# Kernel tuning notes

Hardware: AMD Instinct MI355X
Metric: run time of the kernel (lower is better)

## Reference

```python
import jax, jax.numpy as jnp
import numpy as np

B, S, V = 16, 256, 32000
E, H, L, FFN, NC = 256, 8, 2, 1024, 4
DK = E // H
NQ = E  # n_qubits == hidden_dim == embed_dim (required by the module's shape constraints)
EPS = 1e-5


def qproj(x, theta):
    # Analytic simulation of: RX(x_k) encode + trainable RX(theta_k) + CNOT ladder + MeasureAll(PauliZ).
    # RX gates on the same wire compose; CNOT ladder maps Z_j -> Z_0...Z_j in Heisenberg picture, so
    # <Z_j> = prod_{k<=j} cos(x_k + theta_k)  (product state expectation).
    return jnp.cumprod(jnp.cos(x + theta), axis=-1)


def layernorm(x, g, b):
    m = x.mean(-1, keepdims=True)
    v = x.var(-1, keepdims=True)
    return (x - m) * jax.lax.rsqrt(v + EPS) * g + b


def sinusoidal_pe(seq, d):
    pos = jnp.arange(seq, dtype=jnp.float32)[:, None]
    div = jnp.exp(jnp.arange(0, d, 2, dtype=jnp.float32) * (-np.log(10000.0) / d))
    pe = jnp.zeros((seq, d), jnp.float32)
    pe = pe.at[:, 0::2].set(jnp.sin(pos * div)).at[:, 1::2].set(jnp.cos(pos * div))
    return pe


def _forward(x, token_emb, lstm_W, lstm_b, lstm_theta, ln1_g, ln1_b, ln2_g, ln2_b,
             qkv_theta, combine_W, combine_b, ffn_theta, lin1_W, lin1_b, lin2_W, lin2_b,
             cls_W, cls_b):
    emb = token_emb[x]  # (B, S, E)

    # --- QLSTM: each gate = linear -> quantum circuit -> nonlinearity ---
    def step(carry, xt):
        hx, cx = carry
        comb = jnp.concatenate([xt, hx], axis=-1)                      # (B, 2E)
        z = jnp.einsum('bd,gdq->gbq', comb, lstm_W) + lstm_b[:, None]  # (4, B, NQ)
        q = jnp.cumprod(jnp.cos(z + lstm_theta[:, None, :]), axis=-1)
        f = jax.nn.sigmoid(q[0])
        i = jax.nn.sigmoid(q[1])
        g = jnp.tanh(q[2])
        o = jax.nn.sigmoid(q[3])
        cx = f * cx + i * g
        hx = o * jnp.tanh(cx)
        return (hx, cx), hx

    h0 = jnp.zeros((emb.shape[0], NQ), emb.dtype)
    _, hs = jax.lax.scan(step, (h0, h0), jnp.swapaxes(emb, 0, 1))
    h = jnp.swapaxes(hs, 0, 1)  # (B, S, NQ)

    h = h + sinusoidal_pe(h.shape[1], E)[None]

    # --- quantum transformer blocks ---
    def heads(t):
        return t.reshape(t.shape[0], t.shape[1], H, DK).transpose(0, 2, 1, 3)

    for l in range(L):
        q = qproj(h, qkv_theta[l, 0])
        k = qproj(h, qkv_theta[l, 1])
        v = qproj(h, qkv_theta[l, 2])
        qh, kh, vh = heads(q), heads(k), heads(v)
        scores = jnp.einsum('bhqd,bhkd->bhqk', qh, kh) / jnp.sqrt(jnp.float32(DK))
        attn = jax.nn.softmax(scores, axis=-1)
        out = jnp.einsum('bhqk,bhkd->bhqd', attn, vh).transpose(0, 2, 1, 3).reshape(h.shape)
        out = out @ combine_W[l] + combine_b[l]
        h = layernorm(h + out, ln1_g[l], ln1_b[l])
        ff = qproj(h, ffn_theta[l]) @ lin1_W[l] + lin1_b[l]
        ff = jax.nn.relu(ff) @ lin2_W[l] + lin2_b[l]
        h = layernorm(h + ff, ln2_g[l], ln2_b[l])

    pooled = h.mean(axis=1)  # (B, E)
    return pooled @ cls_W + cls_b  # (B, NC)


def setup_inputs() -> dict:
    key = jax.random.key(0)
    ks = jax.random.split(key, 10)
    s = 0.05
    return {
        'x': jax.random.randint(ks[0], (B, S), 0, V),
        'token_emb': jax.random.normal(ks[1], (V, E), jnp.float32) * s,
        'lstm_W': jax.random.normal(ks[2], (4, 2 * E, NQ), jnp.float32) * s,
        'lstm_b': jnp.zeros((4, NQ), jnp.float32),
        'lstm_theta': jax.random.normal(ks[3], (4, NQ), jnp.float32) * s,
        'ln1_g': jnp.ones((L, E), jnp.float32),
        'ln1_b': jnp.zeros((L, E), jnp.float32),
        'ln2_g': jnp.ones((L, E), jnp.float32),
        'ln2_b': jnp.zeros((L, E), jnp.float32),
        'qkv_theta': jax.random.normal(ks[4], (L, 3, E), jnp.float32) * s,
        'combine_W': jax.random.normal(ks[5], (L, E, E), jnp.float32) * s,
        'combine_b': jnp.zeros((L, E), jnp.float32),
        'ffn_theta': jax.random.normal(ks[6], (L, E), jnp.float32) * s,
        'lin1_W': jax.random.normal(ks[7], (L, E, FFN), jnp.float32) * s,
        'lin1_b': jnp.zeros((L, FFN), jnp.float32),
        'lin2_W': jax.random.normal(ks[8], (L, FFN, E), jnp.float32) * s,
        'lin2_b': jnp.zeros((L, E), jnp.float32),
        'cls_W': jax.random.normal(ks[9], (E, NC), jnp.float32) * s,
        'cls_b': jnp.zeros((NC,), jnp.float32),
    }


def reference(x, token_emb, lstm_W, lstm_b, lstm_theta, ln1_g, ln1_b, ln2_g, ln2_b,
              qkv_theta, combine_W, combine_b, ffn_theta, lin1_W, lin1_b, lin2_W, lin2_b,
              cls_W, cls_b):
    return _forward(x, token_emb, lstm_W, lstm_b, lstm_theta, ln1_g, ln1_b, ln2_g, ln2_b,
                    qkv_theta, combine_W, combine_b, ffn_theta, lin1_W, lin1_b, lin2_W, lin2_b,
                    cls_W, cls_b)
```

## Files before the change

kernel.cpp:

```cpp
#include <hip/hip_runtime.h>
#include <hip/hip_bf16.h>


typedef __attribute__((ext_vector_type(8))) short bf8v;
typedef __attribute__((ext_vector_type(4))) float f4v;
#define MFMA16 __builtin_amdgcn_mfma_f32_16x16x32_bf16

__device__ __forceinline__ unsigned short f2bf(float f) {
  unsigned u = __builtin_bit_cast(unsigned, f);
  u += 0x7fffu + ((u >> 16) & 1u);
  return (unsigned short)(u >> 16);
}
__device__ __forceinline__ float rcp_f(float x) { return __builtin_amdgcn_rcpf(x); }
__device__ __forceinline__ float sigm(float x) { return rcp_f(1.f + __expf(-x)); }
__device__ __forceinline__ float tanh_f(float x) { return 1.f - 2.f * rcp_f(__expf(2.f * x) + 1.f); }

#define DOT2BF(acc, a, b) \
  asm("v_dot2_f32_bf16 %0, %1, %2, %0" : "+v"(acc) : "v"(a), "v"(b))

__global__ void embed_kernel(const int* __restrict__ x, const float* __restrict__ tab,
                             unsigned short* __restrict__ eb) {
  int tok = blockIdx.x, tid = threadIdx.x;
  eb[tok * 256 + tid] = f2bf(tab[x[tok] * 256 + tid]);
}

__global__ void pack_bt(const float* __restrict__ W, int K, int N,
                        unsigned short* __restrict__ Th, long wz, long tz) {
  __shared__ float tile[64][65];
  W += (long)blockIdx.z * wz;
  Th += (long)blockIdx.z * tz;
  int n0 = blockIdx.x * 64, k0 = blockIdx.y * 64;
  int tid = threadIdx.x, tx = tid & 63, ty = tid >> 6;
  for (int r = ty; r < 64; r += 4) tile[r][tx] = W[(k0 + r) * N + n0 + tx];
  __syncthreads();
  for (int r = ty; r < 64; r += 4) {
    Th[(n0 + r) * K + k0 + tx] = f2bf(tile[tx][r]);
  }
}

__global__ void pack_wreg_kernel(const float* __restrict__ lstmW, unsigned* __restrict__ Wreg) {
  int o = blockIdx.x * 256 + threadIdx.x;
  int c = o & 3;
  int q = (o >> 2) & 255;
  int i4 = (o >> 10) & 7;
  int s = (o >> 13) & 3;
  int gi = o >> 15;
  int d = s * 64 + 2 * (i4 * 4 + c);
  unsigned lo = f2bf(lstmW[(gi * 512 + 256 + d) * 256 + q]);
  unsigned hi = f2bf(lstmW[(gi * 512 + 256 + d + 1) * 256 + q]);
  Wreg[o] = lo | (hi << 16);
}

__global__ void pack_wl_kernel(const float* __restrict__ lstmW, unsigned* __restrict__ WLg) {
  int o = blockIdx.x * 256 + threadIdx.x;
  int c = o & 3;
  int q = (o >> 2) & 255;
  int p4 = o >> 10;
  int d = 2 * (p4 * 4 + c);
  unsigned lo = f2bf(lstmW[(3 * 512 + 256 + d) * 256 + q]);
  unsigned hi = f2bf(lstmW[(3 * 512 + 256 + d + 1) * 256 + q]);
  WLg[o] = lo | (hi << 16);
}

__global__ void __launch_bounds__(256) gemm_mfma(const unsigned short* __restrict__ A,
                                                 const unsigned short* __restrict__ B,
                                                 const float* __restrict__ bias,
                                                 float* __restrict__ Cf,
                                                 unsigned short* __restrict__ Cb,
                                                 int M, int N, int K, int mode) {
  __shared__ unsigned short As[128 * 40];
  __shared__ unsigned short Bs[128 * 40];

  const int tid = threadIdx.x;
  const int lane = tid & 63;
  const int wid = tid >> 6;
  const int wr = wid >> 1, wc = wid & 1;
  const int bm = blockIdx.y * 128, bn = blockIdx.x * 128;

  const int srow = tid >> 2;
  const int scol = (tid & 3) * 8;

  f4v acc[4][4] = {};

  for (int kt = 0; kt < K; kt += 32) {
#pragma unroll
    for (int p = 0; p < 2; ++p) {
      int r = srow + p * 64;
      *(uint4*)(&As[r * 40 + scol]) = *(const uint4*)(&A[(bm + r) * K + kt + scol]);
      *(uint4*)(&Bs[r * 40 + scol]) = *(const uint4*)(&B[(bn + r) * K + kt + scol]);
    }
    __syncthreads();

    bf8v a[4], b[4];
    const int kq = (lane >> 4) * 8;
#pragma unroll
    for (int f = 0; f < 4; ++f) {
      a[f] = *(const bf8v*)(&As[(wr * 64 + f * 16 + (lane & 15)) * 40 + kq]);
      b[f] = *(const bf8v*)(&Bs[(wc * 64 + f * 16 + (lane & 15)) * 40 + kq]);
    }
#pragma unroll
    for (int fm = 0; fm < 4; ++fm)
#pragma unroll
      for (int fn = 0; fn < 4; ++fn)
        acc[fm][fn] = MFMA16(a[fm], b[fn], acc[fm][fn], 0, 0, 0);
    __syncthreads();
  }

#pragma unroll
  for (int fm = 0; fm < 4; ++fm)
#pragma unroll
    for (int fn = 0; fn < 4; ++fn) {
      int c = bn + wc * 64 + fn * 16 + (lane & 15);
      int r0 = bm + wr * 64 + fm * 16 + ((lane >> 4) << 2);
      float bv = bias[c];
#pragma unroll
      for (int j = 0; j < 4; ++j) {
        float v = acc[fm][fn][j] + bv;
        if (mode == 1) {
          Cb[(r0 + j) * N + c] = f2bf(fmaxf(v, 0.f));
        } else {
          Cf[(r0 + j) * N + c] = v;
        }
      }
    }
}

__global__ void __launch_bounds__(1024, 4) lstm_kernel(const unsigned* __restrict__ Wreg,
                                                       const unsigned* __restrict__ WLg,
                                                       const float* __restrict__ lstmTh,
                                                       const float* __restrict__ xw,
                                                       float* __restrict__ hb) {
  extern __shared__ char smem[];
  unsigned* WL = (unsigned*)smem;
  float* part = (float*)(smem + 131072);
  float* qv = part + 4096;
  float* wtot = qv + 1024;
  unsigned* hp = (unsigned*)(wtot + 16);

  const int t = threadIdx.x;
  const int b = blockIdx.x;
  const int q = t & 255;
  const int s = t >> 8;
  const int lane = t & 63;
  const int w = t >> 6;

  {
    const uint4* src = (const uint4*)WLg;
    uint4* dst = (uint4*)WL;
    for (int j = t; j < 8192; j += 1024) dst[j] = src[j];
  }
  const uint4* Wreg4 = (const uint4*)Wreg;
  uint4 wreg[24];
#pragma unroll
  for (int j = 0; j < 24; ++j) {
    int gi = j >> 3, i4 = j & 7;
    wreg[j] = Wreg4[((gi * 4 + s) * 8 + i4) * 256 + q];
  }
  const float th = lstmTh[t];
  float cx = 0.f;
  if (t < 128) hp[t] = 0u;
  __syncthreads();

  const int xbase = (b << 8) * 1024;
  const uint4* WL4 = (const uint4*)WL;
  const uint4* hp4 = (const uint4*)hp;

  for (int st = 0; st < 256; ++st) {
    float xv = xw[xbase + st * 1024 + t];

    float a0 = 0.f, a1 = 0.f, a2 = 0.f, a3 = 0.f;
#pragma unroll
    for (int i4 = 0; i4 < 8; ++i4) {
      uint4 hh = hp4[(s << 3) + i4];
      uint4 w3 = WL4[((s << 3) + i4) * 256 + q];
      uint4 w0 = wreg[i4];
      uint4 w1 = wreg[8 + i4];
      uint4 w2 = wreg[16 + i4];
      DOT2BF(a0, w0.x, hh.x); DOT2BF(a0, w0.y, hh.y);
      DOT2BF(a0, w0.z, hh.z); DOT2BF(a0, w0.w, hh.w);
      DOT2BF(a1, w1.x, hh.x); DOT2BF(a1, w1.y, hh.y);
      DOT2BF(a1, w1.z, hh.z); DOT2BF(a1, w1.w, hh.w);
      DOT2BF(a2, w2.x, hh.x); DOT2BF(a2, w2.y, hh.y);
      DOT2BF(a2, w2.z, hh.z); DOT2BF(a2, w2.w, hh.w);
      DOT2BF(a3, w3.x, hh.x); DOT2BF(a3, w3.y, hh.y);
      DOT2BF(a3, w3.z, hh.z); DOT2BF(a3, w3.w, hh.w);
    }
    part[(0 * 4 + s) * 256 + q] = a0;
    part[(1 * 4 + s) * 256 + q] = a1;
    part[(2 * 4 + s) * 256 + q] = a2;
    part[(3 * 4 + s) * 256 + q] = a3;
    __syncthreads();

    float z = part[(s * 4 + 0) * 256 + q] + part[(s * 4 + 1) * 256 + q] +
              part[(s * 4 + 2) * 256 + q] + part[(s * 4 + 3) * 256 + q] + xv + th;
    float v = __cosf(z);

#pragma unroll
    for (int off = 1; off < 64; off <<= 1) {
      float o = __shfl_up(v, off, 64);
      if (lane >= off) v *= o;
    }
    if (lane == 63) wtot[w] = v;
    __syncthreads();
    {
      float p = 1.f;
      int w0g = w & ~3;
      for (int k = w0g; k < w; ++k) p *= wtot[k];
      v *= p;
    }
    qv[t] = v;
    __syncthreads();

    if (t < 256) {
      float fg = sigm(qv[t]);
      float ig = sigm(qv[256 + t]);
      float gg = tanh_f(qv[512 + t]);
      float og = sigm(qv[768 + t]);
      cx = fg * cx + ig * gg;
      float hv = og * tanh_f(cx);
      hb[((b << 8) + st) * 256 + t] = hv;
      float nb = __shfl_xor(hv, 1, 64);
      if ((t & 1) == 0) hp[t >> 1] = (unsigned)f2bf(hv) | ((unsigned)f2bf(nb) << 16);
    }
    __syncthreads();
  }
}

__global__ void pe_add_kernel(float* __restrict__ h) {
  int tok = blockIdx.x, tid = threadIdx.x;
  int s = tok & 255;
  int j = tid >> 1;
  float div = __expf((float)j * -0.07195578415622253f);
  float ang = (float)s * div;
  float pe = (tid & 1) ? __cosf(ang) : __sinf(ang);
  h[tok * 256 + tid] += pe;
}

__global__ void qproj3_kernel(const float* __restrict__ hin, const float* __restrict__ thetas,
                              float* __restrict__ outbase) {
  __shared__ float wtot[4];
  int tok = blockIdx.x, y = blockIdx.y;
  int tid = threadIdx.x, lane = tid & 63, wid = tid >> 6;
  const float* theta = thetas + y * 256;
  float* out = outbase + (long)y * 1048576;
  float v = __cosf(hin[tok * 256 + tid] + theta[tid]);
#pragma unroll
  for (int off = 1; off < 64; off <<= 1) {
    float o = __shfl_up(v, off, 64);
    if (lane >= off) v *= o;
  }
  if (lane == 63) wtot[wid] = v;
  __syncthreads();
  float pre = 1.f;
  for (int w = 0; w < wid; ++w) pre *= wtot[w];
  out[tok * 256 + tid] = v * pre;
}

__global__ void qproj_bf_kernel(const float* __restrict__ hin, const float* __restrict__ theta,
                                unsigned short* __restrict__ outb) {
  __shared__ float wtot[4];
  int tok = blockIdx.x, tid = threadIdx.x, lane = tid & 63, wid = tid >> 6;
  float v = __cosf(hin[tok * 256 + tid] + theta[tid]);
#pragma unroll
  for (int off = 1; off < 64; off <<= 1) {
    float o = __shfl_up(v, off, 64);
    if (lane >= off) v *= o;
  }
  if (lane == 63) wtot[wid] = v;
  __syncthreads();
  float pre = 1.f;
  for (int w = 0; w < wid; ++w) pre *= wtot[w];
  outb[tok * 256 + tid] = f2bf(v * pre);
}

__global__ void __launch_bounds__(256, 1) attn_kernel(const float* __restrict__ qb,
                                                      const float* __restrict__ kb,
                                                      const float* __restrict__ vb,
                                                      unsigned short* __restrict__ outb) {
  extern __shared__ float sm[];
  float* Qs = sm;
  float* Ks = Qs + 256 * 33;
  float* Vs = Ks + 256 * 33;
  float* ps = Vs + 256 * 33;
  int hd = blockIdx.x, b = blockIdx.y;
  int tid = threadIdx.x, lane = tid & 63, wid = tid >> 6;
  const float scale = 0.17677669529663687f;

  for (int i = tid; i < 256 * 32; i += 256) {
    int r = i >> 5, d = i & 31;
    int src = (b * 256 + r) * 256 + hd * 32 + d;
    Qs[r * 33 + d] = qb[src];
    Ks[r * 33 + d] = kb[src];
    Vs[r * 33 + d] = vb[src];
  }
  __syncthreads();

  float* pw = ps + wid * 256;
  for (int r = wid; r < 256; r += 4) {
    float qreg[32];
#pragma unroll
    for (int d = 0; d < 32; ++d) qreg[d] = Qs[r * 33 + d];
    float s[4];
#pragma unroll
    for (int j = 0; j < 4; ++j) {
      int k = lane + 64 * j;
      float a = 0.f;
#pragma unroll
      for (int d = 0; d < 32; ++d) a += qreg[d] * Ks[k * 33 + d];
      s[j] = a * scale;
    }
    float m = fmaxf(fmaxf(s[0], s[1]), fmaxf(s[2], s[3]));
#pragma unroll
    for (int off = 32; off; off >>= 1) m = fmaxf(m, __shfl_xor(m, off, 64));
    float p[4], sum = 0.f;
#pragma unroll
    for (int j = 0; j < 4; ++j) { p[j] = __expf(s[j] - m); sum += p[j]; }
#pragma unroll
    for (int off = 32; off; off >>= 1) sum += __shfl_xor(sum, off, 64);
    float inv = rcp_f(sum);
#pragma unroll
    for (int j = 0; j < 4; ++j) pw[lane + 64 * j] = p[j] * inv;
    int d = lane & 31, half = lane >> 5;
    float a = 0.f;
#pragma unroll 8
    for (int i2 = 0; i2 < 128; ++i2) {
      int k = half * 128 + i2;
      a += pw[k] * Vs[k * 33 + d];
    }
    a += __shfl_down(a, 32, 64);
    if (lane < 32) outb[(b * 256 + r) * 256 + hd * 32 + d] = f2bf(a);
  }
}

__global__ void ln_kernel(float* __restrict__ hio, const float* __restrict__ delta,
                          const float* __restrict__ gamma, const float* __restrict__ beta) {
  __shared__ float red[16];
  int tok = blockIdx.x, tid = threadIdx.x, lane = tid & 63, wid = tid >> 6;
  float v = hio[tok * 256 + tid] + delta[tok * 256 + tid];
  float s1 = v, s2 = v * v;
#pragma unroll
  for (int off = 32; off; off >>= 1) {
    s1 += __shfl_xor(s1, off, 64);
    s2 += __shfl_xor(s2, off, 64);
  }
  if (lane == 0) { red[wid] = s1; red[wid + 8] = s2; }
  __syncthreads();
  float t1 = red[0] + red[1] + red[2] + red[3];
  float t2 = red[8] + red[9] + red[10] + red[11];
  float mean = t1 * (1.f / 256.f);
  float var = t2 * (1.f / 256.f) - mean * mean;
  float w = rsqrtf(var + 1e-5f);
  hio[tok * 256 + tid] = (v - mean) * w * gamma[tid] + beta[tid];
}

__global__ void pool_cls_kernel(const float* __restrict__ h, const float* __restrict__ clsW,
                                const float* __restrict__ clsb, float* __restrict__ out) {
  __shared__ float pl[256];
  __shared__ float red[8];
  int b = blockIdx.x, tid = threadIdx.x, lane = tid & 63, wid = tid >> 6;
  float s = 0.f;
  for (int t = 0; t < 256; ++t) s += h[(b * 256 + t) * 256 + tid];
  pl[tid] = s * (1.f / 256.f);
  __syncthreads();
  for (int c = 0; c < 4; ++c) {
    float v = pl[tid] * clsW[tid * 4 + c];
#pragma unroll
    for (int off = 32; off; off >>= 1) v += __shfl_xor(v, off, 64);
    if (lane == 0) red[wid] = v;
    __syncthreads();
    if (tid == 0) out[b * 4 + c] = red[0] + red[1] + red[2] + red[3] + clsb[c];
    __syncthreads();
  }
}

extern "C" void kernel_launch(void* const* d_in, const int* in_sizes, int n_in,
                              void* d_out, int out_size, void* d_ws, size_t ws_size,
                              hipStream_t stream) {
  const int* x = (const int*)d_in[0];
  const float* token_emb = (const float*)d_in[1];
  const float* lstm_W = (const float*)d_in[2];
  const float* lstm_b = (const float*)d_in[3];
  const float* lstm_th = (const float*)d_in[4];
  const float* ln1_g = (const float*)d_in[5];
  const float* ln1_b = (const float*)d_in[6];
  const float* ln2_g = (const float*)d_in[7];
  const float* ln2_b = (const float*)d_in[8];
  const float* qkv_th = (const float*)d_in[9];
  const float* comb_W = (const float*)d_in[10];
  const float* comb_b = (const float*)d_in[11];
  const float* ffn_th = (const float*)d_in[12];
  const float* lin1_W = (const float*)d_in[13];
  const float* lin1_b = (const float*)d_in[14];
  const float* lin2_W = (const float*)d_in[15];
  const float* lin2_b = (const float*)d_in[16];
  const float* cls_W = (const float*)d_in[17];
  const float* cls_b = (const float*)d_in[18];

  float* ws = (float*)d_ws;
  typedef unsigned short ushort_t;
  ushort_t* emb_b = (ushort_t*)ws;
  ushort_t* att_b = emb_b;
  float* xw = ws + 1048576;
  ushort_t* ffh_b = (ushort_t*)xw;
  float* hb = ws + 5242880;
  float* qq = ws + 6291456;
  float* kk = ws + 7340032;
  float* vv = ws + 8388608;
  float* tmp = ws + 9437184;
  unsigned* Wreg = (unsigned*)tmp;
  unsigned* WLg = (unsigned*)(tmp + 98304);
  ushort_t* ffq_b = (ushort_t*)(ws + 10485760);
  ushort_t* wxt_b = (ushort_t*)(ws + 11534336);
  ushort_t* cmb_b = wxt_b + 262144;
  ushort_t* l1_b = cmb_b + 131072;
  ushort_t* l2_b = l1_b + 524288;

  const int LSTM_LDS = 131072 + 16384 + 4096 + 64 + 512;
  const int ATT_LDS = (3 * 256 * 33 + 4 * 256) * 4;
  (void)hipFuncSetAttribute(reinterpret_cast<const void*>(lstm_kernel),
                            hipFuncAttributeMaxDynamicSharedMemorySize, LSTM_LDS);
  (void)hipFuncSetAttribute(reinterpret_cast<const void*>(attn_kernel),
                            hipFuncAttributeMaxDynamicSharedMemorySize, ATT_LDS);

  embed_kernel<<<4096, 256, 0, stream>>>(x, token_emb, emb_b);
  pack_wreg_kernel<<<384, 256, 0, stream>>>(lstm_W, Wreg);
  pack_wl_kernel<<<128, 256, 0, stream>>>(lstm_W, WLg);
  pack_bt<<<dim3(4, 4, 4), 256, 0, stream>>>(lstm_W, 256, 256, wxt_b, 131072, 65536);
  pack_bt<<<dim3(4, 4, 2), 256, 0, stream>>>(comb_W, 256, 256, cmb_b, 65536, 65536);
  pack_bt<<<dim3(16, 4, 2), 256, 0, stream>>>(lin1_W, 256, 1024, l1_b, 262144, 262144);
  pack_bt<<<dim3(4, 16, 2), 256, 0, stream>>>(lin2_W, 1024, 256, l2_b, 262144, 262144);

  gemm_mfma<<<dim3(8, 32), 256, 0, stream>>>(emb_b, wxt_b, lstm_b,
                                             xw, nullptr, 4096, 1024, 256, 0);
  lstm_kernel<<<16, 1024, LSTM_LDS, stream>>>(Wreg, WLg, lstm_th, xw, hb);
  pe_add_kernel<<<4096, 256, 0, stream>>>(hb);

  for (int l = 0; l < 2; ++l) {
    qproj3_kernel<<<dim3(4096, 3), 256, 0, stream>>>(hb, qkv_th + l * 768, qq);
    attn_kernel<<<dim3(8, 16), 256, ATT_LDS, stream>>>(qq, kk, vv, att_b);
    gemm_mfma<<<dim3(2, 32), 256, 0, stream>>>(att_b, cmb_b + l * 65536, comb_b + l * 256,
                                               tmp, nullptr, 4096, 256, 256, 0);
    ln_kernel<<<4096, 256, 0, stream>>>(hb, tmp, ln1_g + l * 256, ln1_b + l * 256);
    qproj_bf_kernel<<<4096, 256, 0, stream>>>(hb, ffn_th + l * 256, ffq_b);
    gemm_mfma<<<dim3(8, 32), 256, 0, stream>>>(ffq_b, l1_b + l * 262144, lin1_b + l * 1024,
                                               nullptr, ffh_b, 4096, 1024, 256, 1);
    gemm_mfma<<<dim3(2, 32), 256, 0, stream>>>(ffh_b, l2_b + l * 262144, lin2_b + l * 256,
                                               tmp, nullptr, 4096, 256, 1024, 0);
    ln_kernel<<<4096, 256, 0, stream>>>(hb, tmp, ln2_g + l * 256, ln2_b + l * 256);
  }

  pool_cls_kernel<<<16, 256, 0, stream>>>(hb, cls_W, cls_b, (float*)d_out);
}
```

Before: 1.427 ms.

## Halve LSTM block to 512 threads and vectorize attention LDS access

The recurrent LSTM kernel now runs 512 threads per batch, each holding twice the register-resident recurrent weights (48 uint4) and computing two gate outputs. This cuts the cross-K-slice partial reduction from four slices to two and folds the per-wave cumprod prefix into the gate stage, removing one barrier per timestep. The next step's input projection is prefetched during the current step. The attention kernel pads Q/K rows to 36 floats and transposes V so that dot products use float4 LDS loads. The LSTM change raises register pressure a lot and risks spills.

```diff
diff --git a/kernel.cpp b/kernel.cpp
--- a/kernel.cpp
+++ b/kernel.cpp
@@ -42,10 +42,11 @@
   int o = blockIdx.x * 256 + threadIdx.x;
   int c = o & 3;
   int q = (o >> 2) & 255;
-  int i4 = (o >> 10) & 7;
-  int s = (o >> 13) & 3;
-  int gi = o >> 15;
-  int d = s * 64 + 2 * (i4 * 4 + c);
+  int i4 = (o >> 10) & 15;
+  int gs = o >> 14;
+  int gi = gs >> 1, s = gs & 1;
+  int i = i4 * 4 + c;
+  int d = s * 128 + 2 * i;
   unsigned lo = f2bf(lstmW[(gi * 512 + 256 + d) * 256 + q]);
   unsigned hi = f2bf(lstmW[(gi * 512 + 256 + d + 1) * 256 + q]);
   Wreg[o] = lo | (hi << 16);
@@ -125,15 +126,17 @@
     }
 }
 
-__global__ void __launch_bounds__(1024, 4) lstm_kernel(const unsigned* __restrict__ Wreg,
-                                                       const unsigned* __restrict__ WLg,
-                                                       const float* __restrict__ lstmTh,
-                                                       const float* __restrict__ xw,
-                                                       float* __restrict__ hb) {
+__global__ void
+__attribute__((amdgpu_flat_work_group_size(512, 512), amdgpu_waves_per_eu(2, 2)))
+lstm_kernel(const unsigned* __restrict__ Wreg,
+            const unsigned* __restrict__ WLg,
+            const float* __restrict__ lstmTh,
+            const float* __restrict__ xw,
+            float* __restrict__ hb) {
   extern __shared__ char smem[];
   unsigned* WL = (unsigned*)smem;
   float* part = (float*)(smem + 131072);
-  float* qv = part + 4096;
+  float* qv = part + 2048;
   float* wtot = qv + 1024;
   unsigned* hp = (unsigned*)(wtot + 16);
 
@@ -147,16 +150,21 @@
   {
     const uint4* src = (const uint4*)WLg;
     uint4* dst = (uint4*)WL;
-    for (int j = t; j < 8192; j += 1024) dst[j] = src[j];
+    for (int j = t; j < 8192; j += 512) dst[j] = src[j];
   }
   const uint4* Wreg4 = (const uint4*)Wreg;
-  uint4 wreg[24];
-#pragma unroll
-  for (int j = 0; j < 24; ++j) {
-    int gi = j >> 3, i4 = j & 7;
-    wreg[j] = Wreg4[((gi * 4 + s) * 8 + i4) * 256 + q];
-  }
-  const float th = lstmTh[t];
+  uint4 wreg[48];
+#pragma unroll
+  for (int j = 0; j < 48; ++j) {
+    int gi = j >> 4, i4 = j & 15;
+    wreg[j] = Wreg4[((gi * 2 + s) * 16 + i4) * 256 + q];
+  }
+#pragma unroll
+  for (int j = 0; j < 48; ++j) {
+    asm volatile("" : "+v"(wreg[j].x), "+v"(wreg[j].y), "+v"(wreg[j].z), "+v"(wreg[j].w));
+  }
+  const float thA = lstmTh[t];
+  const float thB = lstmTh[512 + t];
   float cx = 0.f;
   if (t < 128) hp[t] = 0u;
   __syncthreads();
@@ -165,17 +173,22 @@
   const uint4* WL4 = (const uint4*)WL;
   const uint4* hp4 = (const uint4*)hp;
 
+  float xa = xw[xbase + t];
+  float xb = xw[xbase + 512 + t];
+
   for (int st = 0; st < 256; ++st) {
-    float xv = xw[xbase + st * 1024 + t];
+    int nx = (st < 255) ? st + 1 : 255;
+    float xa_n = xw[xbase + nx * 1024 + t];
+    float xb_n = xw[xbase + nx * 1024 + 512 + t];
 
     float a0 = 0.f, a1 = 0.f, a2 = 0.f, a3 = 0.f;
 #pragma unroll
-    for (int i4 = 0; i4 < 8; ++i4) {
-      uint4 hh = hp4[(s << 3) + i4];
-      uint4 w3 = WL4[((s << 3) + i4) * 256 + q];
+    for (int i4 = 0; i4 < 16; ++i4) {
+      uint4 hh = hp4[(s << 4) + i4];
+      uint4 w3 = WL4[((s << 4) + i4) * 256 + q];
       uint4 w0 = wreg[i4];
-      uint4 w1 = wreg[8 + i4];
-      uint4 w2 = wreg[16 + i4];
+      uint4 w1 = wreg[16 + i4];
+      uint4 w2 = wreg[32 + i4];
       DOT2BF(a0, w0.x, hh.x); DOT2BF(a0, w0.y, hh.y);
       DOT2BF(a0, w0.z, hh.z); DOT2BF(a0, w0.w, hh.w);
       DOT2BF(a1, w1.x, hh.x); DOT2BF(a1, w1.y, hh.y);
@@ -185,37 +198,41 @@
       DOT2BF(a3, w3.x, hh.x); DOT2BF(a3, w3.y, hh.y);
       DOT2BF(a3, w3.z, hh.z); DOT2BF(a3, w3.w, hh.w);
     }
-    part[(0 * 4 + s) * 256 + q] = a0;
-    part[(1 * 4 + s) * 256 + q] = a1;
-    part[(2 * 4 + s) * 256 + q] = a2;
-    part[(3 * 4 + s) * 256 + q] = a3;
-    __syncthreads();
-
-    float z = part[(s * 4 + 0) * 256 + q] + part[(s * 4 + 1) * 256 + q] +
-              part[(s * 4 + 2) * 256 + q] + part[(s * 4 + 3) * 256 + q] + xv + th;
-    float v = __cosf(z);
-
+    part[(0 * 2 + s) * 256 + q] = a0;
+    part[(1 * 2 + s) * 256 + q] = a1;
+    part[(2 * 2 + s) * 256 + q] = a2;
+    part[(3 * 2 + s) * 256 + q] = a3;
+    __syncthreads();
+
+    int gA = s, gB = s + 2;
+    float zA = part[(gA * 2 + 0) * 256 + q] + part[(gA * 2 + 1) * 256 + q] + xa + thA;
+    float zB = part[(gB * 2 + 0) * 256 + q] + part[(gB * 2 + 1) * 256 + q] + xb + thB;
+    float vA = __cosf(zA);
+    float vB = __cosf(zB);
 #pragma unroll
     for (int off = 1; off < 64; off <<= 1) {
-      float o = __shfl_up(v, off, 64);
-      if (lane >= off) v *= o;
-    }
-    if (lane == 63) wtot[w] = v;
-    __syncthreads();
-    {
-      float p = 1.f;
-      int w0g = w & ~3;
-      for (int k = w0g; k < w; ++k) p *= wtot[k];
-      v *= p;
-    }
-    qv[t] = v;
+      float oA = __shfl_up(vA, off, 64);
+      float oB = __shfl_up(vB, off, 64);
+      if (lane >= off) { vA *= oA; vB *= oB; }
+    }
+    if (lane == 63) { wtot[w * 2] = vA; wtot[w * 2 + 1] = vB; }
+    qv[s * 256 + q] = vA;
+    qv[512 + s * 256 + q] = vB;
     __syncthreads();
 
     if (t < 256) {
-      float fg = sigm(qv[t]);
-      float ig = sigm(qv[256 + t]);
-      float gg = tanh_f(qv[512 + t]);
-      float og = sigm(qv[768 + t]);
+      int j = q >> 6;
+      float p0 = 1.f, p1 = 1.f, p2 = 1.f, p3 = 1.f;
+      for (int k = 0; k < j; ++k) {
+        p0 *= wtot[2 * k];
+        p1 *= wtot[2 * (4 + k)];
+        p2 *= wtot[2 * k + 1];
+        p3 *= wtot[2 * (4 + k) + 1];
+      }
+      float fg = sigm(qv[t] * p0);
+      float ig = sigm(qv[256 + t] * p1);
+      float gg = tanh_f(qv[512 + t] * p2);
+      float og = sigm(qv[768 + t] * p3);
       cx = fg * cx + ig * gg;
       float hv = og * tanh_f(cx);
       hb[((b << 8) + st) * 256 + t] = hv;
@@ -223,6 +240,8 @@
       if ((t & 1) == 0) hp[t >> 1] = (unsigned)f2bf(hv) | ((unsigned)f2bf(nb) << 16);
     }
     __syncthreads();
+    xa = xa_n;
+    xb = xb_n;
   }
 }
 
@@ -279,9 +298,9 @@
                                                       unsigned short* __restrict__ outb) {
   extern __shared__ float sm[];
   float* Qs = sm;
-  float* Ks = Qs + 256 * 33;
-  float* Vs = Ks + 256 * 33;
-  float* ps = Vs + 256 * 33;
+  float* Ks = Qs + 256 * 36;
+  float* Vs = Ks + 256 * 36;
+  float* ps = Vs + 32 * 260;
   int hd = blockIdx.x, b = blockIdx.y;
   int tid = threadIdx.x, lane = tid & 63, wid = tid >> 6;
   const float scale = 0.17677669529663687f;
@@ -289,24 +308,29 @@
   for (int i = tid; i < 256 * 32; i += 256) {
     int r = i >> 5, d = i & 31;
     int src = (b * 256 + r) * 256 + hd * 32 + d;
-    Qs[r * 33 + d] = qb[src];
-    Ks[r * 33 + d] = kb[src];
-    Vs[r * 33 + d] = vb[src];
+    Qs[r * 36 + d] = qb[src];
+    Ks[r * 36 + d] = kb[src];
+    Vs[d * 260 + r] = vb[src];
   }
   __syncthreads();
 
   float* pw = ps + wid * 256;
   for (int r = wid; r < 256; r += 4) {
-    float qreg[32];
-#pragma unroll
-    for (int d = 0; d < 32; ++d) qreg[d] = Qs[r * 33 + d];
+    float4 qreg[8];
+    const float4* qrow = (const float4*)(Qs + r * 36);
+#pragma unroll
+    for (int i = 0; i < 8; ++i) qreg[i] = qrow[i];
     float s[4];
 #pragma unroll
     for (int j = 0; j < 4; ++j) {
       int k = lane + 64 * j;
+      const float4* kr = (const float4*)(Ks + k * 36);
       float a = 0.f;
 #pragma unroll
-      for (int d = 0; d < 32; ++d) a += qreg[d] * Ks[k * 33 + d];
+      for (int i = 0; i < 8; ++i) {
+        float4 kv = kr[i];
+        a += qreg[i].x * kv.x + qreg[i].y * kv.y + qreg[i].z * kv.z + qreg[i].w * kv.w;
+      }
       s[j] = a * scale;
     }
     float m = fmaxf(fmaxf(s[0], s[1]), fmaxf(s[2], s[3]));
@@ -321,11 +345,14 @@
 #pragma unroll
     for (int j = 0; j < 4; ++j) pw[lane + 64 * j] = p[j] * inv;
     int d = lane & 31, half = lane >> 5;
+    const float4* pv = (const float4*)(pw + half * 128);
+    const float4* v4 = (const float4*)(Vs + d * 260 + half * 128);
     float a = 0.f;
-#pragma unroll 8
-    for (int i2 = 0; i2 < 128; ++i2) {
-      int k = half * 128 + i2;
-      a += pw[k] * Vs[k * 33 + d];
+#pragma unroll
+    for (int i = 0; i < 32; ++i) {
+      float4 pp = pv[i];
+      float4 vv = v4[i];
+      a += pp.x * vv.x + pp.y * vv.y + pp.z * vv.z + pp.w * vv.w;
     }
     a += __shfl_down(a, 32, 64);
     if (lane < 32) outb[(b * 256 + r) * 256 + hd * 32 + d] = f2bf(a);
@@ -415,8 +442,8 @@
   ushort_t* l1_b = cmb_b + 131072;
   ushort_t* l2_b = l1_b + 524288;
 
-  const int LSTM_LDS = 131072 + 16384 + 4096 + 64 + 512;
-  const int ATT_LDS = (3 * 256 * 33 + 4 * 256) * 4;
+  const int LSTM_LDS = 131072 + 8192 + 4096 + 64 + 512;
+  const int ATT_LDS = (256 * 36 * 2 + 32 * 260 + 4 * 256) * 4;
   (void)hipFuncSetAttribute(reinterpret_cast<const void*>(lstm_kernel),
                             hipFuncAttributeMaxDynamicSharedMemorySize, LSTM_LDS);
   (void)hipFuncSetAttribute(reinterpret_cast<const void*>(attn_kernel),
@@ -432,7 +459,7 @@
 
   gemm_mfma<<<dim3(8, 32), 256, 0, stream>>>(emb_b, wxt_b, lstm_b,
                                              xw, nullptr, 4096, 1024, 256, 0);
-  lstm_kernel<<<16, 1024, LSTM_LDS, stream>>>(Wreg, WLg, lstm_th, xw, hb);
+  lstm_kernel<<<16, 512, LSTM_LDS, stream>>>(Wreg, WLg, lstm_th, xw, hb);
   pe_add_kernel<<<4096, 256, 0, stream>>>(hb);
 
   for (int l = 0; l < 2; ++l) {
```

Result: faster. 1.273 ms (-10.8%).
